# Performance work log

Measured on AMD Instinct MI355X. Metric: run time of the kernel, lower is better.

Reference implementation:

```python
import jax, jax.numpy as jnp
import numpy as np

N = 4096   # num_nodes
D = 128    # hidden_dim
B = 128    # batch of sequential events
Q = 5      # num_neg_samples


def _linear_params(key, fan_in, fan_out):
    kw, kb = jax.random.split(key)
    lim = 1.0 / np.sqrt(fan_in)
    W = jax.random.uniform(kw, (fan_out, fan_in), minval=-lim, maxval=lim, dtype=jnp.float32)
    b = jax.random.uniform(kb, (fan_out,), minval=-lim, maxval=lim, dtype=jnp.float32)
    return W, b


def setup_inputs() -> dict:
    key = jax.random.key(0)
    ks = jax.random.split(key, 16)
    u = jax.random.randint(ks[0], (B,), 0, N)
    v = jax.random.randint(ks[1], (B,), 0, N)
    event_types = jax.random.randint(ks[2], (B,), 0, 2)
    time_diff = jax.random.uniform(ks[3], (B, 2, 4), dtype=jnp.float32) * 100.0
    neg = jax.random.randint(ks[4], (B, 2 * Q), 0, N)
    z0 = jax.random.normal(ks[5], (N, D), dtype=jnp.float32) * 0.1
    # sparse binary adjacency, avg degree ~32; S = row-normalized attention init
    A = (jax.random.uniform(ks[6], (N, N)) < 32.0 / N).astype(jnp.float32)
    S = A / (A.sum(axis=1, keepdims=True) + 1e-7)
    w_om0, b_om0 = _linear_params(ks[7], 2 * D, 1)
    w_om1, b_om1 = _linear_params(ks[8], 2 * D, 1)
    W_h, b_h = _linear_params(ks[9], D, D)
    W_struct, b_struct = _linear_params(ks[10], D, D)
    W_rec, b_rec = _linear_params(ks[11], D, D)
    W_t, b_t = _linear_params(ks[12], 4, D)
    psi = 0.5 * jnp.ones(2, dtype=jnp.float32)
    return dict(u=u, v=v, event_types=event_types, time_diff=time_diff, neg=neg,
                z0=z0, A=A, S=S,
                w_om0=w_om0, b_om0=b_om0, w_om1=w_om1, b_om1=b_om1, psi=psi,
                W_h=W_h, b_h=b_h, W_struct=W_struct, b_struct=b_struct,
                W_rec=W_rec, b_rec=b_rec, W_t=W_t, b_t=b_t)


def reference(u, v, event_types, time_diff, neg, z0, A, S,
              w_om0, b_om0, w_om1, b_om1, psi,
              W_h, b_h, W_struct, b_struct, W_rec, b_rec, W_t, b_t):
    # time feature normalization (constants from forward())
    t_sd = jnp.array([50.0, 7.0, 15.0, 15.0], dtype=time_diff.dtype)
    td = time_diff / t_sd  # mean is 0

    def intensity(zu, zv, et):
        # lambda = psi_et * softplus(g_et / psi_et), g_et = omega_et([zu; zv])
        x = jnp.concatenate([zu, zv], axis=-1)
        g0 = (x @ w_om0.T + b_om0)[..., 0]
        g1 = (x @ w_om1.T + b_om1)[..., 0]
        g = jnp.where(et == 1, g1, g0)
        p = psi[et]
        return p * jax.nn.softplus(g / (p + 1e-7))

    def step(z, ev):
        ui, vi, tdi, negi = ev
        zu, zv = z[ui], z[vi]                      # gathers on evolving state
        un, vn = negi[Q:], negi[:Q]
        # negative pairs: (u, v_neg[q]) and (u_neg[q], v)
        u_emb = jnp.concatenate([jnp.broadcast_to(zu, (Q, D)), z[un]], axis=0)  # [2Q,D]
        v_emb = jnp.concatenate([z[vn], jnp.broadcast_to(zv, (Q, D))], axis=0)  # [2Q,D]
        # structural update: node u aggregates over v's neighborhood and vice versa
        Whz = z @ W_h.T + b_h                      # [N,D]

        def agg(other):
            m = A[other] > 0                       # [N] neighbor mask
            q = jnp.exp(S[other]) * m
            q = q / (q.sum() + 1e-7)
            sig = jax.nn.sigmoid(q[:, None] * Whz)  # [N,D]
            return jnp.where(m[:, None], sig, 0.0).max(axis=0)  # zeros if no neighbor

        h_struct = jnp.stack([agg(vi), agg(ui)])   # [2,D]
        z_pair = jnp.stack([zu, zv])               # [2,D]
        z_upd = jax.nn.sigmoid(h_struct @ W_struct.T + b_struct
                               + z_pair @ W_rec.T + b_rec
                               + tdi @ W_t.T + b_t)
        z = z.at[ui].set(z_upd[0]).at[vi].set(z_upd[1])
        return z, (zu, zv, u_emb, v_emb)

    z_final, (ZU, ZV, UN, VN) = jax.lax.scan(step, z0, (u, v, td, neg))
    lam_pos = intensity(ZU, ZV, event_types)       # [B]
    et0 = jnp.zeros(UN.shape[:2], dtype=jnp.int32)
    lam_neg = intensity(UN, VN, et0) + intensity(UN, VN, et0 + 1)  # [B,2Q]
    return jnp.concatenate([lam_pos[:, None], lam_neg], axis=1)    # [B, 1+2Q]
```

## Files before the change

### kernel.cpp

```cpp
#include <hip/hip_runtime.h>

#define NN 4096
#define DD 128
#define BB 128
#define QQ 5
#define MAXDEG 96
#define SRCF 0x40000000
#define HP 136
#define FP 132
#define CCAP 1024

typedef __attribute__((ext_vector_type(8))) short bf16x8;
typedef __attribute__((ext_vector_type(4))) float f32x4;

#define LBAR() do { asm volatile("s_waitcnt lgkmcnt(0)" ::: "memory"); \
                    __builtin_amdgcn_sched_barrier(0); \
                    __builtin_amdgcn_s_barrier(); \
                    __builtin_amdgcn_sched_barrier(0); } while (0)

__device__ __forceinline__ float dot4f(float4 a, float4 b) {
    return a.x*b.x + a.y*b.y + a.z*b.z + a.w*b.w;
}
__device__ __forceinline__ unsigned short bfr(float x) {
    unsigned u = __float_as_uint(x);
    return (unsigned short)((u + 0x7fffu + ((u >> 16) & 1u)) >> 16);
}
__device__ __forceinline__ unsigned int pack2bf(float lo, float hi) {
    return ((unsigned int)bfr(hi) << 16) | (unsigned int)bfr(lo);
}

__global__ void nbr_kernel(const int* __restrict__ u, const int* __restrict__ v,
                           const float* __restrict__ A, const float* __restrict__ S,
                           int* __restrict__ nbr_cnt, int2* __restrict__ nbr_pack)
{
    __shared__ int   lcnt[257];
    __shared__ int   sidx[MAXDEG];
    __shared__ float sq[MAXDEG];
    __shared__ float ssum;
    __shared__ int   stot;

    const int p    = blockIdx.x;
    const int i    = p >> 1;
    const int side = p & 1;
    const int other = (side == 0) ? v[i] : u[i];
    const float* Arow = A + (size_t)other * NN;
    const float* Srow = S + (size_t)other * NN;
    const int tid = threadIdx.x;

    const int base = tid * 16;
    int c0 = 0;
    for (int j = 0; j < 16; ++j) c0 += (Arow[base + j] > 0.0f) ? 1 : 0;
    lcnt[tid] = c0;
    __syncthreads();
    if (tid == 0) {
        int s = 0;
        for (int k = 0; k < 256; ++k) { int c = lcnt[k]; lcnt[k] = s; s += c; }
        stot = s;
    }
    __syncthreads();
    int off = lcnt[tid];
    for (int j = 0; j < 16; ++j) {
        if (Arow[base + j] > 0.0f) {
            if (off < MAXDEG) sidx[off] = base + j;
            ++off;
        }
    }
    __syncthreads();
    int cnt = stot; if (cnt > MAXDEG) cnt = MAXDEG;
    for (int jj = tid; jj < cnt; jj += 256) sq[jj] = expf(Srow[sidx[jj]]);
    __syncthreads();
    if (tid == 0) {
        float s = 0.0f;
        for (int jj = 0; jj < cnt; ++jj) s += sq[jj];
        ssum = s + 1e-7f;
    }
    __syncthreads();
    for (int jj = tid; jj < cnt; jj += 256) {
        int2 pk;
        pk.x = sidx[jj];
        pk.y = __float_as_int(sq[jj] / ssum);
        nbr_pack[p * MAXDEG + jj] = pk;
    }
    if (tid == 0) nbr_cnt[p] = cnt;
}

__global__ __launch_bounds__(512) void whz_init(
    const float* __restrict__ z0, const float* __restrict__ Wh, const float* __restrict__ bh,
    float* __restrict__ Whz0)
{
    const int t   = threadIdx.x;
    const int rep = t & 7;
    const int d0  = t >> 3;
    float4 wh0[4], wh1[4];
    #pragma unroll
    for (int m = 0; m < 4; ++m) {
        wh0[m] = *(const float4*)(Wh + (size_t)d0*DD + rep*16 + m*4);
        wh1[m] = *(const float4*)(Wh + (size_t)(d0+64)*DD + rep*16 + m*4);
    }
    const float bh0 = bh[d0], bh1 = bh[d0+64];
    const int r0 = blockIdx.x * 16;
    for (int r = r0; r < r0 + 16; ++r) {
        const float* zr = z0 + (size_t)r*DD + rep*16;
        float a0 = 0.f, a1 = 0.f;
        #pragma unroll
        for (int m = 0; m < 4; ++m) {
            float4 zz = *(const float4*)(zr + m*4);
            a0 += dot4f(zz, wh0[m]);
            a1 += dot4f(zz, wh1[m]);
        }
        a0 += __shfl_xor(a0,1); a0 += __shfl_xor(a0,2); a0 += __shfl_xor(a0,4);
        a1 += __shfl_xor(a1,1); a1 += __shfl_xor(a1,2); a1 += __shfl_xor(a1,4);
        if (rep == 0) {
            Whz0[(size_t)r*DD + d0]    = a0 + bh0;
            Whz0[(size_t)r*DD + d0+64] = a1 + bh1;
        }
    }
}

__global__ void src_kernel(const int* __restrict__ u, const int* __restrict__ v,
                           const int* __restrict__ neg,
                           int* __restrict__ zsrc, int* __restrict__ negsrc)
{
    const int i = blockIdx.x;
    const int k = threadIdx.x;
    if (k >= 2 + 2*QQ) return;
    const int n = (k == 0) ? u[i] : (k == 1) ? v[i] : neg[i*2*QQ + (k-2)];
    int s = n;
    for (int j = i-1; j >= 0; --j) {
        if (v[j] == n) { s = SRCF | (j*2 + 1); break; }
        if (u[j] == n) { s = SRCF | (j*2 + 0); break; }
    }
    if (k < 2) zsrc[i*2 + k] = s;
    else       negsrc[i*2*QQ + (k-2)] = s;
}

__global__ void prep_kernel(const int* __restrict__ u, const int* __restrict__ v,
                            const int* __restrict__ nbr_cnt, const int2* __restrict__ nbr_pack,
                            const float* __restrict__ Whz0,
                            float* __restrict__ maxpre, int* __restrict__ ncorr,
                            int2* __restrict__ corr_pack)
{
    __shared__ int   su[BB], sv[BB];
    __shared__ int   sidx[MAXDEG];
    __shared__ float sq[MAXDEG];
    __shared__ unsigned char cflag[MAXDEG];
    __shared__ int ccnt;

    const int p   = blockIdx.x;
    const int i   = p >> 1;
    const int tid = threadIdx.x;
    if (tid < BB) { su[tid] = u[tid]; sv[tid] = v[tid]; }
    if (tid == 0) ccnt = 0;
    const int cnt = nbr_cnt[p];
    for (int jj = tid; jj < cnt; jj += 128) {
        int2 pk = nbr_pack[p*MAXDEG + jj];
        sidx[jj] = pk.x; sq[jj] = __int_as_float(pk.y);
    }
    __syncthreads();
    for (int jj = tid; jj < cnt; jj += 128) {
        const int r = sidx[jj];
        int fs = -1;
        for (int j = i-1; j >= 0; --j) {
            if (sv[j] == r) { fs = j*2 + 1; break; }
            if (su[j] == r) { fs = j*2 + 0; break; }
        }
        if (fs >= 0) {
            const int pos = atomicAdd(&ccnt, 1);
            int2 cp; cp.x = fs; cp.y = __float_as_int(sq[jj]);
            corr_pack[p*MAXDEG + pos] = cp;
            cflag[jj] = 1;
        } else cflag[jj] = 0;
    }
    __syncthreads();
    const int d = tid;
    float m = -3.0e38f;
    for (int jj = 0; jj < cnt; ++jj)
        if (!cflag[jj]) m = fmaxf(m, sq[jj] * Whz0[(size_t)sidx[jj]*DD + d]);
    maxpre[(size_t)p*DD + d] = m;
    if (tid == 0) ncorr[p] = ccnt;
}

__global__ void pair_kernel(const int* __restrict__ zsrc, const int* __restrict__ ncorr,
                            const int2* __restrict__ corr_pack, int* __restrict__ pdep)
{
    const int g = blockIdx.x;
    const int tid = threadIdx.x;
    const int Astep = 2*g, Bstep = 2*g+1;
    __shared__ int dep;
    if (tid == 0) dep = 0;
    __syncthreads();
    if (tid < 2) {
        const int s = zsrc[Bstep*2 + tid];
        if ((s & SRCF) && (((s & 0xFFFF) >> 1) == Astep)) atomicOr(&dep, 1);
    }
    for (int k = 0; k < 2; ++k) {
        const int p = Bstep*2 + k;
        const int nc = ncorr[p];
        for (int c = tid; c < nc; c += 64)
            if ((corr_pack[p*MAXDEG + c].x >> 1) == Astep) atomicOr(&dep, 1);
    }
    __syncthreads();
    if (tid == 0) pdep[g] = dep;
}

__global__ void compact_kernel(const int* __restrict__ ncorr, const int2* __restrict__ corr_pack,
                               int* __restrict__ corr_off, int2* __restrict__ corr_compact)
{
    __shared__ int off_s[257];
    const int tid = threadIdx.x;
    if (tid == 0) {
        int s = 0;
        for (int p = 0; p < 2*BB; ++p) { off_s[p] = s; s += ncorr[p]; }
        off_s[2*BB] = s;
    }
    __syncthreads();
    corr_off[tid] = off_s[tid];
    if (tid == 0) corr_off[2*BB] = off_s[2*BB];
    const int p = tid;
    const int b0 = off_s[p];
    const int nc = off_s[p+1] - b0;
    for (int c = 0; c < nc; ++c)
        corr_compact[b0 + c] = corr_pack[p*MAXDEG + c];
}

__global__ __launch_bounds__(512) void scan_kernel(
    const float* __restrict__ z0, const float* __restrict__ time_diff,
    const int* __restrict__ nbr_cnt, const int* __restrict__ ncorr,
    const int* __restrict__ corr_off, const int2* __restrict__ corr_compact,
    const float* __restrict__ maxpre, const int* __restrict__ zsrc,
    const int* __restrict__ pdep,
    const float* __restrict__ Wh,  const float* __restrict__ bh,
    const float* __restrict__ Wst, const float* __restrict__ bst,
    const float* __restrict__ Wrc, const float* __restrict__ brc,
    const float* __restrict__ Wt,  const float* __restrict__ bt,
    float* __restrict__ zlog)
{
    __shared__ __align__(16) unsigned short whz_sb[2*BB*DD];
    __shared__ __align__(16) unsigned short zlog_sb[2*BB*DD];
    __shared__ __align__(16) unsigned short h_b[4][HP];
    __shared__ __align__(16) unsigned short zrow_b[4][HP];
    __shared__ __align__(16) unsigned short zupdb[4][HP];
    __shared__ __align__(16) float zupd_s[4][FP];
    __shared__ __align__(16) float tdw_s[4][FP];
    __shared__ __align__(16) float tdi_s[BB*8];
    __shared__ __align__(16) int2 corr_lds[CCAP];
    __shared__ int corr_off_s[2*BB + 1];
    __shared__ int cnt_s[2*BB], zsrc_s[2*BB];
    __shared__ int pdep_s[BB/2];
    __shared__ int defflag[4];

    const int t    = threadIdx.x;
    const int wv   = t >> 6;
    const int ln   = t & 63;
    const int arow = wv*16 + (ln & 15);
    const int kgrp = ln >> 4;
    const int ncol = ln & 15;
    const int dbase = wv*16 + kgrp*4;

    bf16x8 afw[8];
    #pragma unroll
    for (int kt = 0; kt < 8; ++kt) {
        const int kb = kt*32 + kgrp*8;
        const float* src = (kb < 128) ? (Wst + (size_t)arow*DD + kb)
                                      : (Wrc + (size_t)arow*DD + (kb - 128));
        #pragma unroll
        for (int j = 0; j < 8; ++j) afw[kt][j] = (short)bfr(src[j]);
    }
    bf16x8 afh[4];
    #pragma unroll
    for (int kt = 0; kt < 4; ++kt) {
        const float* src = Wh + (size_t)arow*DD + kt*32 + kgrp*8;
        #pragma unroll
        for (int j = 0; j < 8; ++j) afh[kt][j] = (short)bfr(src[j]);
    }
    f32x4 bsv, bhv;
    #pragma unroll
    for (int r = 0; r < 4; ++r) {
        bsv[r] = bst[dbase+r] + brc[dbase+r] + bt[dbase+r];
        bhv[r] = bh[dbase+r];
    }
    const float4 wtA = *(const float4*)(Wt + (size_t)(ln*2)*4);
    const float4 wtB = *(const float4*)(Wt + (size_t)(ln*2+1)*4);

    if (t < 256)      { cnt_s[t] = nbr_cnt[t]; }
    else              { zsrc_s[t-256] = zsrc[t-256]; }
    if (t < BB/2)     pdep_s[t] = pdep[t];
    if (t < 4)        defflag[t] = 0;
    for (int e = t; e < 2*BB + 1; e += 512) corr_off_s[e] = corr_off[e];
    {
        const int ctotal = corr_off[2*BB];
        const int ctot = (ctotal < CCAP) ? ctotal : CCAP;
        for (int e = t; e < ctot; e += 512) corr_lds[e] = corr_compact[e];
    }
    {
        const float sdv[4] = {50.f, 7.f, 15.f, 15.f};
        for (int e = t; e < BB*8; e += 512) tdi_s[e] = time_diff[e] / sdv[e & 3];
    }
    __syncthreads();

    float2 mwork = make_float2(0.f, 0.f);
    float2 mnext = make_float2(0.f, 0.f);
    int2 de0, de1, de2, de3; int ndefr = 0;
    int2 ie0, ie1;           int nintra = 0;
    float2 zn2 = make_float2(0.f, 0.f);

    auto DO_P1 = [&]() {
        const int cc = (ncol < 4) ? ncol : 0;
        const unsigned short* hp = &h_b[cc][0];
        const unsigned short* zp = &zrow_b[cc][0];
        f32x4 accA = {0.f,0.f,0.f,0.f}, accB = {0.f,0.f,0.f,0.f};
        __builtin_amdgcn_s_setprio(1);
        #pragma unroll
        for (int kt = 0; kt < 4; kt += 2) {
            bf16x8 b0 = *(const bf16x8*)&hp[kt*32 + kgrp*8];
            bf16x8 b1 = *(const bf16x8*)&hp[(kt+1)*32 + kgrp*8];
            accA = __builtin_amdgcn_mfma_f32_16x16x32_bf16(afw[kt],   b0, accA, 0,0,0);
            accB = __builtin_amdgcn_mfma_f32_16x16x32_bf16(afw[kt+1], b1, accB, 0,0,0);
        }
        #pragma unroll
        for (int kt = 4; kt < 8; kt += 2) {
            bf16x8 b0 = *(const bf16x8*)&zp[(kt-4)*32 + kgrp*8];
            bf16x8 b1 = *(const bf16x8*)&zp[(kt-3)*32 + kgrp*8];
            accA = __builtin_amdgcn_mfma_f32_16x16x32_bf16(afw[kt],   b0, accA, 0,0,0);
            accB = __builtin_amdgcn_mfma_f32_16x16x32_bf16(afw[kt+1], b1, accB, 0,0,0);
        }
        __builtin_amdgcn_s_setprio(0);
        if (ncol < 4) {
            const f32x4 tdwv = *(const f32x4*)&tdw_s[ncol][dbase];
            f32x4 zu4;
            #pragma unroll
            for (int r = 0; r < 4; ++r) {
                const float a = accA[r] + accB[r] + bsv[r] + tdwv[r];
                zu4[r] = 1.0f/(1.0f + __expf(-a));
            }
            *(f32x4*)&zupd_s[ncol][dbase] = zu4;
            uint2 pk;
            pk.x = pack2bf(zu4[0], zu4[1]);
            pk.y = pack2bf(zu4[2], zu4[3]);
            *(uint2*)&zupdb[ncol][dbase] = pk;
        }
    };

    auto DO_P2 = [&](int writeAll, int G) {
        const int cc = (ncol < 4) ? ncol : 0;
        const unsigned short* up = &zupdb[cc][0];
        f32x4 accA = {0.f,0.f,0.f,0.f}, accB = {0.f,0.f,0.f,0.f};
        __builtin_amdgcn_s_setprio(1);
        {
            bf16x8 b0 = *(const bf16x8*)&up[0*32 + kgrp*8];
            bf16x8 b1 = *(const bf16x8*)&up[1*32 + kgrp*8];
            bf16x8 b2 = *(const bf16x8*)&up[2*32 + kgrp*8];
            bf16x8 b3 = *(const bf16x8*)&up[3*32 + kgrp*8];
            accA = __builtin_amdgcn_mfma_f32_16x16x32_bf16(afh[0], b0, accA, 0,0,0);
            accB = __builtin_amdgcn_mfma_f32_16x16x32_bf16(afh[1], b1, accB, 0,0,0);
            accA = __builtin_amdgcn_mfma_f32_16x16x32_bf16(afh[2], b2, accA, 0,0,0);
            accB = __builtin_amdgcn_mfma_f32_16x16x32_bf16(afh[3], b3, accB, 0,0,0);
        }
        __builtin_amdgcn_s_setprio(0);
        if (ncol < 4 && (writeAll || ncol < 2)) {
            const int row = 4*G + ncol;
            uint2 wpk;
            wpk.x = pack2bf(accA[0]+accB[0]+bhv[0], accA[1]+accB[1]+bhv[1]);
            wpk.y = pack2bf(accA[2]+accB[2]+bhv[2], accA[3]+accB[3]+bhv[3]);
            *(uint2*)&whz_sb[row*DD + dbase] = wpk;
            const f32x4 zu4 = *(const f32x4*)&zupd_s[ncol][dbase];
            uint2 zpk;
            zpk.x = pack2bf(zu4[0], zu4[1]);
            zpk.y = pack2bf(zu4[2], zu4[3]);
            *(uint2*)&zlog_sb[row*DD + dbase] = zpk;
        }
    };

    auto PREP = [&](int curG) {
        const int C = 2*curG + 2;
        if (C >= BB) return;
        if (wv < 4) {
            const int step = C + (wv >> 1);
            const int side = wv & 1;
            const int p1 = step*2 + side;
            const int cbase = corr_off_s[p1];
            const int nc = corr_off_s[p1+1] - cbase;
            float2 m = mnext;
            int nd = 0, ni = 0;
            int2 dl0, dl1, dl2, dl3, il0, il1;
            for (int c = 0; c < nc; ++c) {
                const int idx = cbase + c;
                const int2 e = (idx < CCAP) ? corr_lds[idx] : corr_compact[idx];
                if ((e.x >> 2) == curG) {
                    if (nd==0) dl0=e; else if (nd==1) dl1=e; else if (nd==2) dl2=e; else dl3=e;
                    ++nd;
                } else if ((e.x >> 1) == C && step == C+1) {
                    if (ni==0) il0=e; else il1=e;
                    ++ni;
                } else {
                    const float qc = __int_as_float(e.y);
                    const unsigned pk = *(const unsigned*)&whz_sb[e.x*DD + ln*2];
                    m.x = fmaxf(m.x, qc * __uint_as_float(pk << 16));
                    m.y = fmaxf(m.y, qc * __uint_as_float(pk & 0xffff0000u));
                }
            }
            mwork = m; ndefr = nd; nintra = ni;
            de0=dl0; de1=dl1; de2=dl2; de3=dl3; ie0=il0; ie1=il1;
            if (nd == 0 && ni == 0) {
                float h0 = 0.f, h1 = 0.f;
                if (cnt_s[p1] > 0) {
                    h0 = 1.0f/(1.0f + __expf(-m.x));
                    h1 = 1.0f/(1.0f + __expf(-m.y));
                }
                *(unsigned*)&h_b[wv][ln*2] = pack2bf(h0, h1);
            }
            if (ln == 0) defflag[wv] = nd;
            const int Cn = C + 2;
            const int stepn = (Cn + (wv>>1) < BB) ? (Cn + (wv>>1)) : step;
            const int pn = stepn*2 + side;
            mnext = *(const float2*)&maxpre[(size_t)pn*DD + ln*2];
        } else {
            const int k = wv - 4;
            const int step = C + (k >> 1);
            const int uvk = k & 1;
            const int s = zsrc_s[step*2 + uvk];
            if (s & SRCF) {
                const int row = s & 0xFFFF;
                const int rg  = row >> 2;
                if (rg == curG) {
                    const float2 zf = *(const float2*)&zupd_s[row & 3][ln*2];
                    *(unsigned*)&zrow_b[k][ln*2] = pack2bf(zf.x, zf.y);
                } else if (rg < curG) {
                    *(unsigned*)&zrow_b[k][ln*2] = *(const unsigned*)&zlog_sb[row*DD + ln*2];
                }
            } else {
                *(unsigned*)&zrow_b[k][ln*2] = pack2bf(zn2.x, zn2.y);
            }
            if (wv == 4) {
                const float* tp = &tdi_s[C*8];
                tdw_s[0][ln*2]   = tp[0]*wtA.x + tp[1]*wtA.y + tp[2]*wtA.z + tp[3]*wtA.w;
                tdw_s[0][ln*2+1] = tp[0]*wtB.x + tp[1]*wtB.y + tp[2]*wtB.z + tp[3]*wtB.w;
                tdw_s[1][ln*2]   = tp[4]*wtA.x + tp[5]*wtA.y + tp[6]*wtA.z + tp[7]*wtA.w;
                tdw_s[1][ln*2+1] = tp[4]*wtB.x + tp[5]*wtB.y + tp[6]*wtB.z + tp[7]*wtB.w;
            } else if (wv == 5) {
                const float* tp = &tdi_s[(C+1)*8];
                tdw_s[2][ln*2]   = tp[0]*wtA.x + tp[1]*wtA.y + tp[2]*wtA.z + tp[3]*wtA.w;
                tdw_s[2][ln*2+1] = tp[0]*wtB.x + tp[1]*wtB.y + tp[2]*wtB.z + tp[3]*wtB.w;
                tdw_s[3][ln*2]   = tp[4]*wtA.x + tp[5]*wtA.y + tp[6]*wtA.z + tp[7]*wtA.w;
                tdw_s[3][ln*2+1] = tp[4]*wtB.x + tp[5]*wtB.y + tp[6]*wtB.z + tp[7]*wtB.w;
            }
            const int Cn = C + 2;
            if (Cn + (k>>1) < BB) {
                const int sn = zsrc_s[(Cn + (k>>1))*2 + uvk];
                if (!(sn & SRCF)) zn2 = *(const float2*)&z0[(size_t)sn*DD + ln*2];
            }
        }
    };

    if (wv < 4) {
        const int p0 = (wv >> 1)*2 + (wv & 1);
        mnext = *(const float2*)&maxpre[(size_t)p0*DD + ln*2];
    } else {
        const int k = wv - 4;
        const int s = zsrc_s[(k >> 1)*2 + (k & 1)];
        if (!(s & SRCF)) zn2 = *(const float2*)&z0[(size_t)s*DD + ln*2];
    }
    PREP(-1);
    LBAR();

    for (int G = 0; G < BB/2; ++G) {
        if (defflag[0] | defflag[1] | defflag[2] | defflag[3]) {
            if (wv < 4 && ndefr) {
                float2 m = mwork;
                {
                    const float qc = __int_as_float(de0.y);
                    const unsigned pk = *(const unsigned*)&whz_sb[de0.x*DD + ln*2];
                    m.x = fmaxf(m.x, qc * __uint_as_float(pk << 16));
                    m.y = fmaxf(m.y, qc * __uint_as_float(pk & 0xffff0000u));
                }
                if (ndefr > 1) {
                    const float qc = __int_as_float(de1.y);
                    const unsigned pk = *(const unsigned*)&whz_sb[de1.x*DD + ln*2];
                    m.x = fmaxf(m.x, qc * __uint_as_float(pk << 16));
                    m.y = fmaxf(m.y, qc * __uint_as_float(pk & 0xffff0000u));
                }
                if (ndefr > 2) {
                    const float qc = __int_as_float(de2.y);
                    const unsigned pk = *(const unsigned*)&whz_sb[de2.x*DD + ln*2];
                    m.x = fmaxf(m.x, qc * __uint_as_float(pk << 16));
                    m.y = fmaxf(m.y, qc * __uint_as_float(pk & 0xffff0000u));
                }
                if (ndefr > 3) {
                    const float qc = __int_as_float(de3.y);
                    const unsigned pk = *(const unsigned*)&whz_sb[de3.x*DD + ln*2];
                    m.x = fmaxf(m.x, qc * __uint_as_float(pk << 16));
                    m.y = fmaxf(m.y, qc * __uint_as_float(pk & 0xffff0000u));
                }
                mwork = m; ndefr = 0;
                if (nintra == 0) {
                    const int p1 = (2*G + (wv>>1))*2 + (wv & 1);
                    float h0 = 0.f, h1 = 0.f;
                    if (cnt_s[p1] > 0) {
                        h0 = 1.0f/(1.0f + __expf(-m.x));
                        h1 = 1.0f/(1.0f + __expf(-m.y));
                    }
                    *(unsigned*)&h_b[wv][ln*2] = pack2bf(h0, h1);
                }
            }
            LBAR();
        }

        if (!pdep_s[G]) {
            DO_P1();
            LBAR();
            DO_P2(1, G);
            PREP(G);
            LBAR();
        } else {
            DO_P1();
            LBAR();
            DO_P2(0, G);
            if (wv >= 6) {
                const int k = wv - 4;
                const int s = zsrc_s[(2*G+1)*2 + (k & 1)];
                if ((s & SRCF) && (((s & 0xFFFF) >> 2) == G)) {
                    const int row = s & 0xFFFF;
                    const float2 zf = *(const float2*)&zupd_s[row & 3][ln*2];
                    *(unsigned*)&zrow_b[k][ln*2] = pack2bf(zf.x, zf.y);
                }
            }
            LBAR();
            if ((wv == 2 || wv == 3) && nintra) {
                float2 m = mwork;
                {
                    const float qc = __int_as_float(ie0.y);
                    const unsigned pk = *(const unsigned*)&whz_sb[ie0.x*DD + ln*2];
                    m.x = fmaxf(m.x, qc * __uint_as_float(pk << 16));
                    m.y = fmaxf(m.y, qc * __uint_as_float(pk & 0xffff0000u));
                }
                if (nintra > 1) {
                    const float qc = __int_as_float(ie1.y);
                    const unsigned pk = *(const unsigned*)&whz_sb[ie1.x*DD + ln*2];
                    m.x = fmaxf(m.x, qc * __uint_as_float(pk << 16));
                    m.y = fmaxf(m.y, qc * __uint_as_float(pk & 0xffff0000u));
                }
                const int p1 = (2*G+1)*2 + (wv & 1);
                float h0 = 0.f, h1 = 0.f;
                if (cnt_s[p1] > 0) {
                    h0 = 1.0f/(1.0f + __expf(-m.x));
                    h1 = 1.0f/(1.0f + __expf(-m.y));
                }
                *(unsigned*)&h_b[wv][ln*2] = pack2bf(h0, h1);
                nintra = 0;
            }
            LBAR();
            DO_P1();
            LBAR();
            DO_P2(1, G);
            PREP(G);
            LBAR();
        }
    }

    for (int e = t; e < BB*DD; e += 512) {
        const unsigned pk = *(const unsigned*)&zlog_sb[e*2];
        float2 val;
        val.x = __uint_as_float(pk << 16);
        val.y = __uint_as_float(pk & 0xffff0000u);
        *(float2*)&zlog[(size_t)e*2] = val;
    }
}

__global__ void lam_kernel(const float* __restrict__ z0, const float* __restrict__ zlog,
                           const int* __restrict__ zsrc, const int* __restrict__ negsrc,
                           const int* __restrict__ et,
                           const float* __restrict__ w0, const float* __restrict__ b0,
                           const float* __restrict__ w1, const float* __restrict__ b1,
                           const float* __restrict__ psi,
                           float* __restrict__ out)
{
    const int b   = blockIdx.x;
    const int i   = b / 11;
    const int col = b % 11;
    const int l   = threadIdx.x;

    auto rp = [&](int s) -> const float* {
        return (s & SRCF) ? (zlog + (size_t)(s & 0xFFFF)*DD) : (z0 + (size_t)s*DD);
    };
    const float* xu;
    const float* xv;
    if (col == 0) { xu = rp(zsrc[i*2]); xv = rp(zsrc[i*2+1]); }
    else {
        const int k = col - 1;
        xu = (k < QQ) ? rp(zsrc[i*2])            : rp(negsrc[i*2*QQ + k]);
        xv = (k < QQ) ? rp(negsrc[i*2*QQ + k])   : rp(zsrc[i*2+1]);
    }
    float g0 = xu[l]*w0[l] + xu[l+64]*w0[l+64] + xv[l]*w0[DD+l] + xv[l+64]*w0[DD+l+64];
    float g1 = xu[l]*w1[l] + xu[l+64]*w1[l+64] + xv[l]*w1[DD+l] + xv[l+64]*w1[DD+l+64];
    #pragma unroll
    for (int s = 32; s >= 1; s >>= 1) { g0 += __shfl_xor(g0, s); g1 += __shfl_xor(g1, s); }
    if (l == 0) {
        g0 += b0[0]; g1 += b1[0];
        const float p0 = psi[0], p1 = psi[1];
        float r;
        if (col == 0) {
            const int e = et[i];
            const float g = e ? g1 : g0;
            const float p = e ? p1 : p0;
            const float y = g / (p + 1e-7f);
            r = p * (fmaxf(y, 0.f) + log1pf(expf(-fabsf(y))));
        } else {
            const float y0 = g0 / (p0 + 1e-7f);
            const float y1 = g1 / (p1 + 1e-7f);
            r = p0 * (fmaxf(y0, 0.f) + log1pf(expf(-fabsf(y0))))
              + p1 * (fmaxf(y1, 0.f) + log1pf(expf(-fabsf(y1))));
        }
        out[i*11 + col] = r;
    }
}

extern "C" void kernel_launch(void* const* d_in, const int* in_sizes, int n_in,
                              void* d_out, int out_size, void* d_ws, size_t ws_size,
                              hipStream_t stream)
{
    const int*   u   = (const int*)d_in[0];
    const int*   v   = (const int*)d_in[1];
    const int*   et  = (const int*)d_in[2];
    const float* td  = (const float*)d_in[3];
    const int*   neg = (const int*)d_in[4];
    const float* z0  = (const float*)d_in[5];
    const float* A   = (const float*)d_in[6];
    const float* S   = (const float*)d_in[7];
    const float* w0  = (const float*)d_in[8];
    const float* b0  = (const float*)d_in[9];
    const float* w1  = (const float*)d_in[10];
    const float* b1  = (const float*)d_in[11];
    const float* psi = (const float*)d_in[12];
    const float* Wh  = (const float*)d_in[13];
    const float* bh  = (const float*)d_in[14];
    const float* Wst = (const float*)d_in[15];
    const float* bst = (const float*)d_in[16];
    const float* Wrc = (const float*)d_in[17];
    const float* brc = (const float*)d_in[18];
    const float* Wt  = (const float*)d_in[19];
    const float* bt  = (const float*)d_in[20];

    char* ws = (char*)d_ws;
    size_t off = 0;
    auto alloc = [&](size_t bytes) {
        void* p = ws + off;
        off = (off + bytes + 255) & ~(size_t)255;
        return p;
    };
    float* Whz0   = (float*)alloc((size_t)NN*DD*sizeof(float));
    float* maxpre = (float*)alloc((size_t)2*BB*DD*sizeof(float));
    float* zlog   = (float*)alloc((size_t)2*BB*DD*sizeof(float));
    int*   ncnt   = (int*)alloc((size_t)2*BB*sizeof(int));
    int*   ncorr  = (int*)alloc((size_t)2*BB*sizeof(int));
    int2*  cpk    = (int2*)alloc((size_t)2*BB*MAXDEG*sizeof(int2));
    int*   zsrc   = (int*)alloc((size_t)2*BB*sizeof(int));
    int*   negsrc = (int*)alloc((size_t)BB*2*QQ*sizeof(int));
    int*   pdep   = (int*)alloc((size_t)(BB/2)*sizeof(int));
    int*   coff   = (int*)alloc((size_t)(2*BB+1)*sizeof(int));
    int2*  ccomp  = (int2*)alloc((size_t)2*BB*MAXDEG*sizeof(int2));
    int2*  npk    = (int2*)alloc((size_t)2*BB*MAXDEG*sizeof(int2));

    whz_init<<<NN/16, 512, 0, stream>>>(z0, Wh, bh, Whz0);
    nbr_kernel<<<2*BB, 256, 0, stream>>>(u, v, A, S, ncnt, npk);
    src_kernel<<<BB, 64, 0, stream>>>(u, v, neg, zsrc, negsrc);
    prep_kernel<<<2*BB, 128, 0, stream>>>(u, v, ncnt, npk, Whz0, maxpre, ncorr, cpk);
    pair_kernel<<<BB/2, 64, 0, stream>>>(zsrc, ncorr, cpk, pdep);
    compact_kernel<<<1, 256, 0, stream>>>(ncorr, cpk, coff, ccomp);
    scan_kernel<<<1, 512, 0, stream>>>(z0, td, ncnt, ncorr, coff, ccomp, maxpre, zsrc, pdep,
                                       Wh, bh, Wst, bst, Wrc, brc, Wt, bt, zlog);
    lam_kernel<<<BB*(1 + 2*QQ), 64, 0, stream>>>(z0, zlog, zsrc, negsrc, et,
                                                 w0, b0, w1, b1, psi, (float*)d_out);
}
```

Measured before the change: 199.8 us.

## Fuse neighbor and prep kernels, move pair and compact logic into scan

Merges nbr_kernel and prep_kernel into one nbrprep kernel so the neighbor list stays in shared memory and is never round-tripped through global memory. The pair-dependency and compaction work moves into the single-block scan kernel, using a wavefront prefix scan and direct reads from corr_pack, which removes two small kernel launches. A separate cnt_kernel recomputes neighbor counts from A. The aim is to cut launch overhead and global traffic, at the cost of extra serial setup inside the scan block and a second read of the A rows. The code also leaves odd leftovers: an empty block, an unused struct, and a block-scope extern declaration of a __global__ function.

```diff
diff --git a/kernel.cpp b/kernel.cpp
--- a/kernel.cpp
+++ b/kernel.cpp
@@ -27,61 +27,6 @@
 }
 __device__ __forceinline__ unsigned int pack2bf(float lo, float hi) {
     return ((unsigned int)bfr(hi) << 16) | (unsigned int)bfr(lo);
-}
-
-__global__ void nbr_kernel(const int* __restrict__ u, const int* __restrict__ v,
-                           const float* __restrict__ A, const float* __restrict__ S,
-                           int* __restrict__ nbr_cnt, int2* __restrict__ nbr_pack)
-{
-    __shared__ int   lcnt[257];
-    __shared__ int   sidx[MAXDEG];
-    __shared__ float sq[MAXDEG];
-    __shared__ float ssum;
-    __shared__ int   stot;
-
-    const int p    = blockIdx.x;
-    const int i    = p >> 1;
-    const int side = p & 1;
-    const int other = (side == 0) ? v[i] : u[i];
-    const float* Arow = A + (size_t)other * NN;
-    const float* Srow = S + (size_t)other * NN;
-    const int tid = threadIdx.x;
-
-    const int base = tid * 16;
-    int c0 = 0;
-    for (int j = 0; j < 16; ++j) c0 += (Arow[base + j] > 0.0f) ? 1 : 0;
-    lcnt[tid] = c0;
-    __syncthreads();
-    if (tid == 0) {
-        int s = 0;
-        for (int k = 0; k < 256; ++k) { int c = lcnt[k]; lcnt[k] = s; s += c; }
-        stot = s;
-    }
-    __syncthreads();
-    int off = lcnt[tid];
-    for (int j = 0; j < 16; ++j) {
-        if (Arow[base + j] > 0.0f) {
-            if (off < MAXDEG) sidx[off] = base + j;
-            ++off;
-        }
-    }
-    __syncthreads();
-    int cnt = stot; if (cnt > MAXDEG) cnt = MAXDEG;
-    for (int jj = tid; jj < cnt; jj += 256) sq[jj] = expf(Srow[sidx[jj]]);
-    __syncthreads();
-    if (tid == 0) {
-        float s = 0.0f;
-        for (int jj = 0; jj < cnt; ++jj) s += sq[jj];
-        ssum = s + 1e-7f;
-    }
-    __syncthreads();
-    for (int jj = tid; jj < cnt; jj += 256) {
-        int2 pk;
-        pk.x = sidx[jj];
-        pk.y = __float_as_int(sq[jj] / ssum);
-        nbr_pack[p * MAXDEG + jj] = pk;
-    }
-    if (tid == 0) nbr_cnt[p] = cnt;
 }
 
 __global__ __launch_bounds__(512) void whz_init(
@@ -134,30 +79,63 @@
     else       negsrc[i*2*QQ + (k-2)] = s;
 }
 
-__global__ void prep_kernel(const int* __restrict__ u, const int* __restrict__ v,
-                            const int* __restrict__ nbr_cnt, const int2* __restrict__ nbr_pack,
-                            const float* __restrict__ Whz0,
-                            float* __restrict__ maxpre, int* __restrict__ ncorr,
-                            int2* __restrict__ corr_pack)
+__global__ void nbrprep_kernel(const int* __restrict__ u, const int* __restrict__ v,
+                               const float* __restrict__ A, const float* __restrict__ S,
+                               const float* __restrict__ Whz0,
+                               float* __restrict__ maxpre, int* __restrict__ ncorr,
+                               int2* __restrict__ corr_pack)
 {
-    __shared__ int   su[BB], sv[BB];
+    __shared__ int   lcnt[257];
     __shared__ int   sidx[MAXDEG];
     __shared__ float sq[MAXDEG];
     __shared__ unsigned char cflag[MAXDEG];
-    __shared__ int ccnt;
-
-    const int p   = blockIdx.x;
-    const int i   = p >> 1;
-    const int tid = threadIdx.x;
+    __shared__ int   su[BB], sv[BB];
+    __shared__ float ssum;
+    __shared__ int   stot, ccnt;
+
+    const int p    = blockIdx.x;
+    const int i    = p >> 1;
+    const int side = p & 1;
+    const int tid  = threadIdx.x;
+
+    const int other = (side == 0) ? v[i] : u[i];
+    const float* Arow = A + (size_t)other * NN;
+    const float* Srow = S + (size_t)other * NN;
+
+    const int base = tid * 16;
+    int c0 = 0;
+    for (int j = 0; j < 16; ++j) c0 += (Arow[base + j] > 0.0f) ? 1 : 0;
+    lcnt[tid] = c0;
     if (tid < BB) { su[tid] = u[tid]; sv[tid] = v[tid]; }
     if (tid == 0) ccnt = 0;
-    const int cnt = nbr_cnt[p];
-    for (int jj = tid; jj < cnt; jj += 128) {
-        int2 pk = nbr_pack[p*MAXDEG + jj];
-        sidx[jj] = pk.x; sq[jj] = __int_as_float(pk.y);
-    }
-    __syncthreads();
-    for (int jj = tid; jj < cnt; jj += 128) {
+    __syncthreads();
+    if (tid == 0) {
+        int s = 0;
+        for (int k = 0; k < 256; ++k) { int c = lcnt[k]; lcnt[k] = s; s += c; }
+        stot = s;
+    }
+    __syncthreads();
+    int off = lcnt[tid];
+    for (int j = 0; j < 16; ++j) {
+        if (Arow[base + j] > 0.0f) {
+            if (off < MAXDEG) sidx[off] = base + j;
+            ++off;
+        }
+    }
+    __syncthreads();
+    const int cnt = (stot < MAXDEG) ? stot : MAXDEG;
+    for (int jj = tid; jj < cnt; jj += 256) sq[jj] = expf(Srow[sidx[jj]]);
+    __syncthreads();
+    if (tid == 0) {
+        float s = 0.0f;
+        for (int jj = 0; jj < cnt; ++jj) s += sq[jj];
+        ssum = s + 1e-7f;
+    }
+    __syncthreads();
+    for (int jj = tid; jj < cnt; jj += 256) sq[jj] = sq[jj] / ssum;
+    __syncthreads();
+
+    for (int jj = tid; jj < cnt; jj += 256) {
         const int r = sidx[jj];
         int fs = -1;
         for (int j = i-1; j >= 0; --j) {
@@ -172,63 +150,23 @@
         } else cflag[jj] = 0;
     }
     __syncthreads();
-    const int d = tid;
-    float m = -3.0e38f;
-    for (int jj = 0; jj < cnt; ++jj)
-        if (!cflag[jj]) m = fmaxf(m, sq[jj] * Whz0[(size_t)sidx[jj]*DD + d]);
-    maxpre[(size_t)p*DD + d] = m;
+
+    if (tid < DD) {
+        const int d = tid;
+        float m = -3.0e38f;
+        for (int jj = 0; jj < cnt; ++jj)
+            if (!cflag[jj]) m = fmaxf(m, sq[jj] * Whz0[(size_t)sidx[jj]*DD + d]);
+        maxpre[(size_t)p*DD + d] = m;
+    }
     if (tid == 0) ncorr[p] = ccnt;
-}
-
-__global__ void pair_kernel(const int* __restrict__ zsrc, const int* __restrict__ ncorr,
-                            const int2* __restrict__ corr_pack, int* __restrict__ pdep)
-{
-    const int g = blockIdx.x;
-    const int tid = threadIdx.x;
-    const int Astep = 2*g, Bstep = 2*g+1;
-    __shared__ int dep;
-    if (tid == 0) dep = 0;
-    __syncthreads();
-    if (tid < 2) {
-        const int s = zsrc[Bstep*2 + tid];
-        if ((s & SRCF) && (((s & 0xFFFF) >> 1) == Astep)) atomicOr(&dep, 1);
-    }
-    for (int k = 0; k < 2; ++k) {
-        const int p = Bstep*2 + k;
-        const int nc = ncorr[p];
-        for (int c = tid; c < nc; c += 64)
-            if ((corr_pack[p*MAXDEG + c].x >> 1) == Astep) atomicOr(&dep, 1);
-    }
-    __syncthreads();
-    if (tid == 0) pdep[g] = dep;
-}
-
-__global__ void compact_kernel(const int* __restrict__ ncorr, const int2* __restrict__ corr_pack,
-                               int* __restrict__ corr_off, int2* __restrict__ corr_compact)
-{
-    __shared__ int off_s[257];
-    const int tid = threadIdx.x;
-    if (tid == 0) {
-        int s = 0;
-        for (int p = 0; p < 2*BB; ++p) { off_s[p] = s; s += ncorr[p]; }
-        off_s[2*BB] = s;
-    }
-    __syncthreads();
-    corr_off[tid] = off_s[tid];
-    if (tid == 0) corr_off[2*BB] = off_s[2*BB];
-    const int p = tid;
-    const int b0 = off_s[p];
-    const int nc = off_s[p+1] - b0;
-    for (int c = 0; c < nc; ++c)
-        corr_compact[b0 + c] = corr_pack[p*MAXDEG + c];
 }
 
 __global__ __launch_bounds__(512) void scan_kernel(
     const float* __restrict__ z0, const float* __restrict__ time_diff,
-    const int* __restrict__ nbr_cnt, const int* __restrict__ ncorr,
-    const int* __restrict__ corr_off, const int2* __restrict__ corr_compact,
+    const int* __restrict__ nbr_cnt_unused, const int* __restrict__ ncorr,
+    const int2* __restrict__ corr_pack,
     const float* __restrict__ maxpre, const int* __restrict__ zsrc,
-    const int* __restrict__ pdep,
+    const int* __restrict__ nbr_cntg,
     const float* __restrict__ Wh,  const float* __restrict__ bh,
     const float* __restrict__ Wst, const float* __restrict__ bst,
     const float* __restrict__ Wrc, const float* __restrict__ brc,
@@ -282,19 +220,63 @@
     const float4 wtA = *(const float4*)(Wt + (size_t)(ln*2)*4);
     const float4 wtB = *(const float4*)(Wt + (size_t)(ln*2+1)*4);
 
-    if (t < 256)      { cnt_s[t] = nbr_cnt[t]; }
+    if (t < 256)      { cnt_s[t] = nbr_cntg[t]; }
     else              { zsrc_s[t-256] = zsrc[t-256]; }
-    if (t < BB/2)     pdep_s[t] = pdep[t];
     if (t < 4)        defflag[t] = 0;
-    for (int e = t; e < 2*BB + 1; e += 512) corr_off_s[e] = corr_off[e];
-    {
-        const int ctotal = corr_off[2*BB];
-        const int ctot = (ctotal < CCAP) ? ctotal : CCAP;
-        for (int e = t; e < ctot; e += 512) corr_lds[e] = corr_compact[e];
-    }
     {
         const float sdv[4] = {50.f, 7.f, 15.f, 15.f};
         for (int e = t; e < BB*8; e += 512) tdi_s[e] = time_diff[e] / sdv[e & 3];
+    }
+    __syncthreads();
+
+    if (wv == 0) {
+        int n0 = ncorr[ln*4+0], n1 = ncorr[ln*4+1], n2 = ncorr[ln*4+2], n3 = ncorr[ln*4+3];
+        int loc = n0 + n1 + n2 + n3;
+        int incl = loc;
+        #pragma unroll
+        for (int s = 1; s < 64; s <<= 1) {
+            int up = __shfl_up(incl, s);
+            if (ln >= s) incl += up;
+        }
+        const int bse = incl - loc;
+        corr_off_s[ln*4+0] = bse;
+        corr_off_s[ln*4+1] = bse + n0;
+        corr_off_s[ln*4+2] = bse + n0 + n1;
+        corr_off_s[ln*4+3] = bse + n0 + n1 + n2;
+        if (ln == 63) corr_off_s[256] = incl;
+    }
+    __syncthreads();
+
+    if (t < 256) {
+        const int b0 = corr_off_s[t];
+        const int nc = corr_off_s[t+1] - b0;
+        for (int c = 0; c < nc; ++c) {
+            const int idx = b0 + c;
+            if (idx < CCAP) corr_lds[idx] = corr_pack[t*MAXDEG + c];
+        }
+    }
+    __syncthreads();
+
+    if (t < BB/2) {
+        const int g = t;
+        int dep = 0;
+        #pragma unroll
+        for (int k = 0; k < 2; ++k) {
+            const int s = zsrc_s[(2*g+1)*2 + k];
+            if ((s & SRCF) && (((s & 0xFFFF) >> 1) == 2*g)) dep = 1;
+        }
+        #pragma unroll
+        for (int k = 0; k < 2; ++k) {
+            const int p = (2*g+1)*2 + k;
+            const int b0 = corr_off_s[p];
+            const int nc = corr_off_s[p+1] - b0;
+            for (int c = 0; c < nc; ++c) {
+                const int idx = b0 + c;
+                const int2 e = (idx < CCAP) ? corr_lds[idx] : corr_pack[p*MAXDEG + c];
+                if ((e.x >> 1) == 2*g) dep = 1;
+            }
+        }
+        pdep_s[g] = dep;
     }
     __syncthreads();
 
@@ -385,7 +367,7 @@
             int2 dl0, dl1, dl2, dl3, il0, il1;
             for (int c = 0; c < nc; ++c) {
                 const int idx = cbase + c;
-                const int2 e = (idx < CCAP) ? corr_lds[idx] : corr_compact[idx];
+                const int2 e = (idx < CCAP) ? corr_lds[idx] : corr_pack[p1*MAXDEG + c];
                 if ((e.x >> 2) == curG) {
                     if (nd==0) dl0=e; else if (nd==1) dl1=e; else if (nd==2) dl2=e; else dl3=e;
                     ++nd;
@@ -655,19 +637,38 @@
     int2*  cpk    = (int2*)alloc((size_t)2*BB*MAXDEG*sizeof(int2));
     int*   zsrc   = (int*)alloc((size_t)2*BB*sizeof(int));
     int*   negsrc = (int*)alloc((size_t)BB*2*QQ*sizeof(int));
-    int*   pdep   = (int*)alloc((size_t)(BB/2)*sizeof(int));
-    int*   coff   = (int*)alloc((size_t)(2*BB+1)*sizeof(int));
-    int2*  ccomp  = (int2*)alloc((size_t)2*BB*MAXDEG*sizeof(int2));
-    int2*  npk    = (int2*)alloc((size_t)2*BB*MAXDEG*sizeof(int2));
 
     whz_init<<<NN/16, 512, 0, stream>>>(z0, Wh, bh, Whz0);
-    nbr_kernel<<<2*BB, 256, 0, stream>>>(u, v, A, S, ncnt, npk);
     src_kernel<<<BB, 64, 0, stream>>>(u, v, neg, zsrc, negsrc);
-    prep_kernel<<<2*BB, 128, 0, stream>>>(u, v, ncnt, npk, Whz0, maxpre, ncorr, cpk);
-    pair_kernel<<<BB/2, 64, 0, stream>>>(zsrc, ncorr, cpk, pdep);
-    compact_kernel<<<1, 256, 0, stream>>>(ncorr, cpk, coff, ccomp);
-    scan_kernel<<<1, 512, 0, stream>>>(z0, td, ncnt, ncorr, coff, ccomp, maxpre, zsrc, pdep,
+    nbrprep_kernel<<<2*BB, 256, 0, stream>>>(u, v, A, S, Whz0, maxpre, ncorr, cpk);
+    {
+    }
+    struct Dummy {};
+    extern __global__ void cnt_kernel(const int*, const int*, const float*, int*);
+    cnt_kernel<<<2*BB, 256, 0, stream>>>(u, v, A, ncnt);
+    scan_kernel<<<1, 512, 0, stream>>>(z0, td, nullptr, ncorr, cpk, maxpre, zsrc, ncnt,
                                        Wh, bh, Wst, bst, Wrc, brc, Wt, bt, zlog);
     lam_kernel<<<BB*(1 + 2*QQ), 64, 0, stream>>>(z0, zlog, zsrc, negsrc, et,
                                                  w0, b0, w1, b1, psi, (float*)d_out);
 }
+
+__global__ void cnt_kernel(const int* __restrict__ u, const int* __restrict__ v,
+                           const float* __restrict__ A, int* __restrict__ ncnt)
+{
+    __shared__ int csum;
+    const int p    = blockIdx.x;
+    const int i    = p >> 1;
+    const int side = p & 1;
+    const int other = (side == 0) ? v[i] : u[i];
+    const float* Arow = A + (size_t)other * NN;
+    const int tid = threadIdx.x;
+    if (tid == 0) csum = 0;
+    __syncthreads();
+    int c0 = 0;
+    for (int j = tid; j < NN; j += 256) c0 += (Arow[j] > 0.0f) ? 1 : 0;
+    c0 += __shfl_xor(c0, 1);  c0 += __shfl_xor(c0, 2);  c0 += __shfl_xor(c0, 4);
+    c0 += __shfl_xor(c0, 8);  c0 += __shfl_xor(c0, 16); c0 += __shfl_xor(c0, 32);
+    if ((tid & 63) == 0) atomicAdd(&csum, c0);
+    __syncthreads();
+    if (tid == 0) ncnt[p] = (csum < MAXDEG) ? csum : MAXDEG;
+}
```

Result: faster. 193.9 us (-2.9%).
